# Optimization experiments

Hardware: AMD Instinct MI355X
Metric: run time of the kernel (lower is better)

Reference implementation:

```python
import jax, jax.numpy as jnp
import numpy as np
import math

B, S, E, H, D, L, HF = 8, 1024, 512, 8, 64, 6, 2048
EPS = 1e-5
INF = 1000000.0


def _gelu(x):
    # custom tanh-approx gelu from the source
    return 0.5 * x * (1 + jnp.tanh(math.sqrt(2 / math.pi) * (x + 0.044715 * x ** 3)))


def _layernorm(x, gamma, beta):
    mean = jnp.mean(x, axis=-1, keepdims=True)
    var = jnp.mean((x - mean) ** 2, axis=-1, keepdims=True)
    return gamma * ((x - mean) / jnp.sqrt(var + EPS)) + beta


def setup_inputs() -> dict:
    key = jax.random.key(0)
    ks = jax.random.split(key, 10)
    scale = 0.02
    x = jax.random.normal(ks[0], (B, S, E), dtype=jnp.float32)
    att_mask = jax.random.randint(ks[1], (B, S), 0, 2) == 1
    WQ = jax.random.normal(ks[2], (L, E, E), dtype=jnp.float32) * scale
    WK = jax.random.normal(ks[3], (L, E, E), dtype=jnp.float32) * scale
    WV = jax.random.normal(ks[4], (L, E, E), dtype=jnp.float32) * scale
    WO = jax.random.normal(ks[5], (L, E, E), dtype=jnp.float32) * scale
    W1 = jax.random.normal(ks[6], (L, HF, E), dtype=jnp.float32) * scale
    W2 = jax.random.normal(ks[7], (L, E, HF), dtype=jnp.float32) * scale
    bQ = jnp.zeros((L, E)); bK = jnp.zeros((L, E)); bV = jnp.zeros((L, E)); bO = jnp.zeros((L, E))
    b1 = jnp.zeros((L, HF)); b2 = jnp.zeros((L, E))
    g1 = jnp.ones((L, E)); bt1 = jnp.zeros((L, E))
    g2 = jnp.ones((L, E)); bt2 = jnp.zeros((L, E))
    return {"x": x, "att_mask": att_mask, "WQ": WQ, "bQ": bQ, "WK": WK, "bK": bK,
            "WV": WV, "bV": bV, "WO": WO, "bO": bO, "W1": W1, "b1": b1, "W2": W2,
            "b2": b2, "g1": g1, "bt1": bt1, "g2": g2, "bt2": bt2}


def reference(x, att_mask, WQ, bQ, WK, bK, WV, bV, WO, bO, W1, b1, W2, b2, g1, bt1, g2, bt2):
    # additive mask applied to scores: score - (~mask) * infinity, broadcast over (B,1,1,S)
    inv_att = (~att_mask).astype(x.dtype)[:, None, None, :] * INF
    inv_sqrt_d = 1.0 / math.sqrt(D)
    for l in range(L):
        # --- multi-head self-attention ---
        q = (jnp.einsum('bse,fe->bsf', x, WQ[l]) + bQ[l]).reshape(B, S, H, D).transpose(0, 2, 1, 3)
        k = (jnp.einsum('bse,fe->bsf', x, WK[l]) + bK[l]).reshape(B, S, H, D).transpose(0, 2, 1, 3)
        v = (jnp.einsum('bse,fe->bsf', x, WV[l]) + bV[l]).reshape(B, S, H, D).transpose(0, 2, 1, 3)
        score = jnp.einsum('bhsd,bhtd->bhst', q, k) * inv_sqrt_d - inv_att
        attn = jax.nn.softmax(score, axis=-1)
        o = jnp.einsum('bhst,bhtd->bhsd', attn, v).transpose(0, 2, 1, 3).reshape(B, S, E)
        o = jnp.einsum('bse,fe->bsf', o, WO[l]) + bO[l]
        x = _layernorm(x + o, g1[l], bt1[l])
        # --- pointwise feed-forward ---
        h = _gelu(jnp.einsum('bse,fe->bsf', x, W1[l]) + b1[l])
        f = jnp.einsum('bsf,ef->bse', h, W2[l]) + b2[l]
        x = _layernorm(x + f, g2[l], bt2[l])
    return x
```

## Files before the change

kernel.cpp:

```cpp
#include <hip/hip_runtime.h>
#include <cstdint>
#include <cstddef>

#define NB 8
#define NS 1024
#define NE 512
#define NH 8
#define ND 64
#define NL 6
#define NHF 2048
#define NROW (NB*NS)

typedef __bf16 bf16_t;
typedef __bf16 bf8v __attribute__((ext_vector_type(8)));
typedef __bf16 bf4v __attribute__((ext_vector_type(4)));
typedef float  f4   __attribute__((ext_vector_type(4)));

extern "C" __device__ float __ocml_native_exp2_f32(float);
#define EXP2F __ocml_native_exp2_f32
#define LOG2E 1.4426950408889634f

__device__ __forceinline__ void async_copy16(const bf16_t* g, bf16_t* l) {
    __builtin_amdgcn_global_load_lds(
        (const __attribute__((address_space(1))) void*)g,
        (__attribute__((address_space(3))) void*)l,
        16, 0, 0);
}

__device__ __forceinline__ float gelu_f(float x) {
    const float s = fmaf(0.044715f * x * x, x, x);
    const float e = EXP2F(-2.3022081995f * s);
    return x * __builtin_amdgcn_rcpf(1.0f + e);
}

template<int BN, int ACT, int OUT>
__device__ __forceinline__ void gemm_core(
    bf16_t* __restrict__ sm,
    const bf16_t* __restrict__ A, const bf16_t* __restrict__ Bm,
    const float* __restrict__ bias, bf16_t* __restrict__ Cb,
    int m0, int n0, int N, int K)
{
    constexpr int JN = BN / 32, WSPAN = BN / 2;
    bf16_t* As = sm;
    bf16_t* Bs = sm + 2*128*64;
    const int tid  = threadIdx.x;
    const int lane = tid & 63;
    const int wave = tid >> 6;
    const int wm = wave >> 1, wn = wave & 1;
    const int quad = lane >> 4, l16 = lane & 15;
    const int srow = tid >> 3;
    const int scol = (((tid & 7) ^ (srow & 7)) << 3);

    f4 acc[4][JN] = {};

    const bf16_t* Ag = A  + (size_t)(m0 + srow) * K + scol;
    const bf16_t* Bg = Bm + (size_t)(n0 + srow) * K + scol;
    const int sw = (l16 & 7);

    auto stage = [&](int buf, int kt) {
#pragma unroll
        for (int r = 0; r < 4; ++r)
            async_copy16(Ag + (size_t)r * 32 * K + kt, As + buf*8192 + tid*8 + r*2048);
#pragma unroll
        for (int r = 0; r < BN/32; ++r)
            async_copy16(Bg + (size_t)r * 32 * K + kt, Bs + buf*(BN*64) + tid*8 + r*2048);
    };

    stage(0, 0);
    int buf = 0;
    for (int kt = 0; kt < K; kt += 64, buf ^= 1) {
        __syncthreads();
        if (kt + 64 < K) stage(buf ^ 1, kt + 64);
        const bf16_t* Ab = As + buf*8192;
        const bf16_t* Bb = Bs + buf*(BN*64);
#pragma unroll
        for (int s = 0; s < 2; ++s) {
            const int c8 = ((s*4 + quad) ^ sw) * 8;
            bf8v af[4], bfv[JN];
#pragma unroll
            for (int i = 0; i < 4; ++i)
                af[i] = *(const bf8v*)(Ab + (wm*64 + i*16 + l16)*64 + c8);
#pragma unroll
            for (int j = 0; j < JN; ++j)
                bfv[j] = *(const bf8v*)(Bb + (wn*WSPAN + j*16 + l16)*64 + c8);
#pragma unroll
            for (int i = 0; i < 4; ++i)
#pragma unroll
                for (int j = 0; j < JN; ++j)
                    acc[i][j] = __builtin_amdgcn_mfma_f32_16x16x32_bf16(bfv[j], af[i], acc[i][j], 0, 0, 0);
        }
    }

#pragma unroll
    for (int i = 0; i < 4; ++i) {
        const int mi = m0 + wm*64 + i*16 + l16;
        const size_t m = (size_t)mi;
#pragma unroll
        for (int j = 0; j < JN; ++j) {
            const int nb = n0 + wn*WSPAN + j*16 + quad*4;
            const f4 bv = *(const f4*)(bias + nb);
            f4 v = acc[i][j] + bv;
            if (ACT) {
#pragma unroll
                for (int r = 0; r < 4; ++r) v[r] = gelu_f(v[r]);
            }
            bf4v* cp = (bf4v*)(Cb + m * (size_t)N + nb);
            bf4v o;
            if (OUT == 2) {
                const bf4v old = *cp;
#pragma unroll
                for (int r = 0; r < 4; ++r) o[r] = (bf16_t)((float)old[r] + v[r]);
            } else {
#pragma unroll
                for (int r = 0; r < 4; ++r) o[r] = (bf16_t)v[r];
            }
            *cp = o;
        }
    }
}

template<int BN, int ACT, int OUT>
__global__ __launch_bounds__(256)
void gemm_bt_k(const bf16_t* __restrict__ A, const bf16_t* __restrict__ Bm,
               const float* __restrict__ bias, bf16_t* __restrict__ Cb, int N, int K)
{
    __shared__ __align__(16) bf16_t smem[2*128*64 + 2*BN*64];
    gemm_core<BN, ACT, OUT>(smem, A, Bm, bias, Cb,
                            blockIdx.x * 128, blockIdx.y * BN, N, K);
}

__global__ __launch_bounds__(512, 2)
void gemm_rmw_ln_k(const bf16_t* __restrict__ A, const bf16_t* __restrict__ Bm,
                   const float* __restrict__ bias, bf16_t* __restrict__ xb,
                   const float* __restrict__ gamma, const float* __restrict__ beta,
                   float* __restrict__ fout, int wf, int K)
{
    __shared__ __align__(16) bf16_t As[2*32*64];
    __shared__ __align__(16) bf16_t Bs[2*512*64];
    __shared__ float wsum[8][32], wssq[8][32];
    const int tid  = threadIdx.x;
    const int lane = tid & 63;
    const int wave = tid >> 6;
    const int quad = lane >> 4, l16 = lane & 15;
    const int sw = l16 & 7;
    const int srow = tid >> 3;
    const int scol = ((tid & 7) ^ (srow & 7)) << 3;
    const int m0 = blockIdx.x * 32;

    const bf16_t* Ag = A  + (size_t)(m0 + srow) * K + scol;
    const bf16_t* Bg = Bm + (size_t)srow * K + scol;

    f4 acc[2][4] = {};

    auto stage = [&](int buf, int kt) {
        if (tid < 256)
            async_copy16(Ag + kt, As + buf*2048 + tid*8);
#pragma unroll
        for (int r = 0; r < 8; ++r)
            async_copy16(Bg + (size_t)r * 64 * K + kt, Bs + buf*32768 + (r*512 + tid)*8);
    };

    stage(0, 0);
    int buf = 0;
    for (int kt = 0; kt < K; kt += 64, buf ^= 1) {
        __syncthreads();
        if (kt + 64 < K) stage(buf ^ 1, kt + 64);
        const bf16_t* Ab = As + buf*2048;
        const bf16_t* Bb = Bs + buf*32768;
#pragma unroll
        for (int s = 0; s < 2; ++s) {
            const int c8 = ((s*4 + quad) ^ sw) * 8;
            bf8v af[2], bfv[4];
#pragma unroll
            for (int i = 0; i < 2; ++i)
                af[i] = *(const bf8v*)(Ab + (i*16 + l16)*64 + c8);
#pragma unroll
            for (int j = 0; j < 4; ++j)
                bfv[j] = *(const bf8v*)(Bb + (wave*64 + j*16 + l16)*64 + c8);
#pragma unroll
            for (int i = 0; i < 2; ++i)
#pragma unroll
                for (int j = 0; j < 4; ++j)
                    acc[i][j] = __builtin_amdgcn_mfma_f32_16x16x32_bf16(bfv[j], af[i], acc[i][j], 0, 0, 0);
        }
    }

    f4 v[2][4];
    float ps[2], pss[2];
#pragma unroll
    for (int i = 0; i < 2; ++i) {
        ps[i] = 0.f; pss[i] = 0.f;
        const size_t m = (size_t)(m0 + i*16 + l16);
#pragma unroll
        for (int j = 0; j < 4; ++j) {
            const int nb = wave*64 + j*16 + quad*4;
            const f4 bv = *(const f4*)(bias + nb);
            const bf4v old = *(const bf4v*)(xb + m * NE + nb);
            f4 t = acc[i][j] + bv;
#pragma unroll
            for (int r = 0; r < 4; ++r) {
                t[r] += (float)old[r];
                ps[i]  += t[r];
                pss[i] += t[r] * t[r];
            }
            v[i][j] = t;
        }
        ps[i]  += __shfl_xor(ps[i], 16, 64);
        ps[i]  += __shfl_xor(ps[i], 32, 64);
        pss[i] += __shfl_xor(pss[i], 16, 64);
        pss[i] += __shfl_xor(pss[i], 32, 64);
    }
    if (quad == 0) {
#pragma unroll
        for (int i = 0; i < 2; ++i) {
            wsum[wave][i*16 + l16] = ps[i];
            wssq[wave][i*16 + l16] = pss[i];
        }
    }
    __syncthreads();
#pragma unroll
    for (int i = 0; i < 2; ++i) {
        const int row = i*16 + l16;
        float s = 0.f, ss = 0.f;
#pragma unroll
        for (int w = 0; w < 8; ++w) { s += wsum[w][row]; ss += wssq[w][row]; }
        const float mean = s * (1.0f / NE);
        const float var  = ss * (1.0f / NE) - mean * mean;
        const float inv  = rsqrtf(var + 1e-5f);
        const size_t m = (size_t)(m0 + row);
#pragma unroll
        for (int j = 0; j < 4; ++j) {
            const int nb = wave*64 + j*16 + quad*4;
            const f4 gm = *(const f4*)(gamma + nb);
            const f4 bt = *(const f4*)(beta + nb);
            f4 o;
            bf4v ob;
#pragma unroll
            for (int r = 0; r < 4; ++r) {
                o[r]  = gm[r] * ((v[i][j][r] - mean) * inv) + bt[r];
                ob[r] = (bf16_t)o[r];
            }
            *(bf4v*)(xb + m * NE + nb) = ob;
            if (wf) *(f4*)(fout + m * NE + nb) = o;
        }
    }
}

__global__ __launch_bounds__(256, 2)
void gemm_qkv_k(const bf16_t* __restrict__ A,
                const bf16_t* __restrict__ wq, const bf16_t* __restrict__ wk, const bf16_t* __restrict__ wv,
                const float* __restrict__ bq, const float* __restrict__ bk, const float* __restrict__ bv,
                bf16_t* __restrict__ Q, bf16_t* __restrict__ K, bf16_t* __restrict__ Vt,
                const unsigned short* __restrict__ rank)
{
    __shared__ __align__(16) bf16_t As_[2*128*64];
    __shared__ __align__(16) bf16_t Bs_[3][2*64*64];
    const int tid  = threadIdx.x;
    const int lane = tid & 63;
    const int wave = tid >> 6;
    const int wm = wave >> 1, wn = wave & 1;
    const int quad = lane >> 4, l16 = lane & 15;
    const int sw = l16 & 7;
    const int srow = tid >> 3;
    const int scol = (((tid & 7) ^ (srow & 7)) << 3);
    const int m0 = blockIdx.x * 128, n0 = blockIdx.y * 64;

    const bf16_t* Ag = A + (size_t)(m0 + srow) * NE + scol;
    const bf16_t* Wg0 = wq + (size_t)(n0 + srow) * NE + scol;
    const bf16_t* Wg1 = wk + (size_t)(n0 + srow) * NE + scol;
    const bf16_t* Wg2 = wv + (size_t)(n0 + srow) * NE + scol;

    f4 acc[3][4][2] = {};

    auto stage = [&](int buf, int kt) {
#pragma unroll
        for (int r = 0; r < 4; ++r)
            async_copy16(Ag + (size_t)r*32*NE + kt, As_ + buf*8192 + tid*8 + r*2048);
#pragma unroll
        for (int r = 0; r < 2; ++r) {
            async_copy16(Wg0 + (size_t)r*32*NE + kt, Bs_[0] + buf*4096 + tid*8 + r*2048);
            async_copy16(Wg1 + (size_t)r*32*NE + kt, Bs_[1] + buf*4096 + tid*8 + r*2048);
            async_copy16(Wg2 + (size_t)r*32*NE + kt, Bs_[2] + buf*4096 + tid*8 + r*2048);
        }
    };

    stage(0, 0);
    int buf = 0;
    for (int kt = 0; kt < NE; kt += 64, buf ^= 1) {
        __syncthreads();
        if (kt + 64 < NE) stage(buf ^ 1, kt + 64);
        const bf16_t* Ab = As_ + buf*8192;
#pragma unroll
        for (int s = 0; s < 2; ++s) {
            const int c8 = ((s*4 + quad) ^ sw) * 8;
            bf8v af[4];
#pragma unroll
            for (int i = 0; i < 4; ++i)
                af[i] = *(const bf8v*)(Ab + (wm*64 + i*16 + l16)*64 + c8);
#pragma unroll
            for (int mat = 0; mat < 3; ++mat) {
                const bf16_t* Bb = Bs_[mat] + buf*4096;
                const bf8v b0 = *(const bf8v*)(Bb + (wn*32      + l16)*64 + c8);
                const bf8v b1 = *(const bf8v*)(Bb + (wn*32 + 16 + l16)*64 + c8);
                if (mat < 2) {
#pragma unroll
                    for (int i = 0; i < 4; ++i) {
                        acc[mat][i][0] = __builtin_amdgcn_mfma_f32_16x16x32_bf16(b0, af[i], acc[mat][i][0], 0, 0, 0);
                        acc[mat][i][1] = __builtin_amdgcn_mfma_f32_16x16x32_bf16(b1, af[i], acc[mat][i][1], 0, 0, 0);
                    }
                } else {
#pragma unroll
                    for (int i = 0; i < 4; ++i) {
                        acc[2][i][0] = __builtin_amdgcn_mfma_f32_16x16x32_bf16(af[i], b0, acc[2][i][0], 0, 0, 0);
                        acc[2][i][1] = __builtin_amdgcn_mfma_f32_16x16x32_bf16(af[i], b1, acc[2][i][1], 0, 0, 0);
                    }
                }
            }
        }
    }

#pragma unroll
    for (int i = 0; i < 4; ++i) {
        const int mi = m0 + wm*64 + i*16 + l16;
        const int mk = (mi & ~1023) + (int)rank[mi];
#pragma unroll
        for (int j = 0; j < 2; ++j) {
            const int nb = n0 + wn*32 + j*16 + quad*4;
            const f4 vq = acc[0][i][j] + *(const f4*)(bq + nb);
            const f4 vk = acc[1][i][j] + *(const f4*)(bk + nb);
            bf4v oq, ok;
#pragma unroll
            for (int r = 0; r < 4; ++r) { oq[r] = (bf16_t)vq[r]; ok[r] = (bf16_t)vk[r]; }
            *(bf4v*)(Q + (size_t)mi * NE + nb) = oq;
            *(bf4v*)(K + (size_t)mk * NE + nb) = ok;
        }
    }
#pragma unroll
    for (int j = 0; j < 2; ++j) {
        const int n = n0 + wn*32 + j*16 + l16;
        const float bvv = bv[n];
#pragma unroll
        for (int i = 0; i < 4; ++i) {
            const int mbase = m0 + wm*64 + i*16 + quad*4;
            const size_t b8h = (size_t)((mbase >> 10)*8 + (n >> 6));
            bf16_t* rowp = Vt + (b8h*64 + (size_t)(n & 63))*1024;
#pragma unroll
            for (int r = 0; r < 4; ++r)
                rowp[rank[mbase + r]] = (bf16_t)(acc[2][i][j][r] + bvv);
        }
    }
}

template<int ACT, int OUT>
__device__ __forceinline__ void gemm256_core(
    bf16_t* __restrict__ sm,
    const bf16_t* __restrict__ A, const bf16_t* __restrict__ Bm,
    const float* __restrict__ bias, bf16_t* __restrict__ Cb,
    int m0, int n0, int N, int K)
{
    const int tid  = threadIdx.x;
    const int lane = tid & 63;
    const int wave = tid >> 6;
    const int wm = wave >> 2, wn = wave & 3;
    const int quad = lane >> 4, l16 = lane & 15;
    const int sw = l16 & 7;
    const int srow = tid >> 3;
    const int scol = ((tid & 7) ^ (srow & 7)) << 3;

    bf16_t* As = sm;
    bf16_t* Bs = sm + 4 * 8192;

    const bf16_t* Ag = A  + (size_t)(m0 + srow) * K + scol;
    const bf16_t* Bg = Bm + (size_t)(n0 + srow) * K + scol;

    auto stageA = [&](int d, int h, int kt) {
        bf16_t* dst = As + (d*2 + h) * 8192 + tid * 8;
        const bf16_t* src = Ag + (size_t)(h * 128) * K + kt;
        async_copy16(src, dst);
        async_copy16(src + (size_t)64 * K, dst + 4096);
    };
    auto stageB = [&](int d, int h, int kt) {
        bf16_t* dst = Bs + (d*2 + h) * 8192 + tid * 8;
        const bf16_t* src = Bg + (size_t)(h * 128) * K + kt;
        async_copy16(src, dst);
        async_copy16(src + (size_t)64 * K, dst + 4096);
    };

    const int nt = K >> 6;

    f4 acc[8][4] = {};
    bf8v bfr[4][2], al[4][2], ah[4][2];

    auto mfmaQ = [&](const bf8v (&af)[4][2], int fb, int gb) {
#pragma unroll
        for (int kh = 0; kh < 2; ++kh)
#pragma unroll
            for (int f = 0; f < 4; ++f)
#pragma unroll
                for (int g = 0; g < 2; ++g)
                    acc[fb+f][gb+g] = __builtin_amdgcn_mfma_f32_16x16x32_bf16(bfr[gb+g][kh], af[f][kh], acc[fb+f][gb+g], 0, 0, 0);
    };

    stageB(0, 0, 0);  stageB(0, 1, 0);  stageA(0, 0, 0);  stageA(0, 1, 0);
    stageB(1, 0, 64); stageB(1, 1, 64); stageA(1, 0, 64);
    asm volatile("s_waitcnt vmcnt(6)" ::: "memory");
    __builtin_amdgcn_s_barrier();

    for (int t = 0; t < nt; ++t) {
        const int d = t & 1;
        const int kt2 = (t + 2) << 6;
        const bf16_t* Ab = As + (d*2 + wm) * 8192;
        const bf16_t* Bb = Bs + (d*2 + (wn >> 1)) * 8192 + (wn & 1) * 4096;

#pragma unroll
        for (int g = 0; g < 4; ++g)
#pragma unroll
            for (int kh = 0; kh < 2; ++kh)
                bfr[g][kh] = *(const bf8v*)(Bb + (g*16 + l16)*64 + (((kh*4 + quad) ^ sw) << 3));
#pragma unroll
        for (int f = 0; f < 4; ++f)
#pragma unroll
            for (int kh = 0; kh < 2; ++kh)
                al[f][kh] = *(const bf8v*)(Ab + (f*16 + l16)*64 + (((kh*4 + quad) ^ sw) << 3));
        if (t + 1 < nt) stageA(d ^ 1, 1, (t + 1) << 6);
        __builtin_amdgcn_s_barrier();
        __builtin_amdgcn_s_setprio(1);
        mfmaQ(al, 0, 0);
        __builtin_amdgcn_s_setprio(0);
        asm volatile("s_waitcnt lgkmcnt(0)" ::: "memory");
        __builtin_amdgcn_s_barrier();

#pragma unroll
        for (int f = 0; f < 4; ++f)
#pragma unroll
            for (int kh = 0; kh < 2; ++kh)
                ah[f][kh] = *(const bf8v*)(Ab + ((f + 4)*16 + l16)*64 + (((kh*4 + quad) ^ sw) << 3));
        if (t + 2 < nt) stageB(d, 0, kt2);
        __builtin_amdgcn_s_barrier();
        __builtin_amdgcn_s_setprio(1);
        mfmaQ(ah, 4, 0);
        __builtin_amdgcn_s_setprio(0);
        asm volatile("s_waitcnt lgkmcnt(0)" ::: "memory");
        __builtin_amdgcn_s_barrier();

        if (t + 2 < nt) stageB(d, 1, kt2);
        __builtin_amdgcn_s_barrier();
        __builtin_amdgcn_s_setprio(1);
        mfmaQ(al, 0, 2);
        __builtin_amdgcn_s_setprio(0);
        asm volatile("s_waitcnt lgkmcnt(0)" ::: "memory");
        __builtin_amdgcn_s_barrier();

        if (t + 2 < nt) stageA(d, 0, kt2);
        __builtin_amdgcn_s_barrier();
        __builtin_amdgcn_s_setprio(1);
        mfmaQ(ah, 4, 2);
        __builtin_amdgcn_s_setprio(0);
        asm volatile("s_waitcnt lgkmcnt(0)" ::: "memory");
        if (t + 1 < nt) {
            if (t + 2 < nt) asm volatile("s_waitcnt vmcnt(6)" ::: "memory");
            else            asm volatile("s_waitcnt vmcnt(0)" ::: "memory");
        }
        __builtin_amdgcn_s_barrier();
    }

#pragma unroll
    for (int f = 0; f < 8; ++f) {
        const int mi = m0 + wm*128 + f*16 + l16;
        const size_t m = (size_t)mi;
#pragma unroll
        for (int g = 0; g < 4; ++g) {
            const int nb = n0 + wn*64 + g*16 + quad*4;
            const f4 bv = *(const f4*)(bias + nb);
            f4 v = acc[f][g] + bv;
            if (ACT) {
#pragma unroll
                for (int r = 0; r < 4; ++r) v[r] = gelu_f(v[r]);
            }
            bf4v* cp = (bf4v*)(Cb + m * (size_t)N + nb);
            bf4v o;
            if (OUT == 2) {
                const bf4v old = *cp;
#pragma unroll
                for (int r = 0; r < 4; ++r) o[r] = (bf16_t)((float)old[r] + v[r]);
            } else {
#pragma unroll
                for (int r = 0; r < 4; ++r) o[r] = (bf16_t)v[r];
            }
            *cp = o;
        }
    }
}

template<int ACT, int OUT>
__global__ __launch_bounds__(512, 2)
void gemm256_k(const bf16_t* __restrict__ A, const bf16_t* __restrict__ Bm,
               const float* __restrict__ bias, bf16_t* __restrict__ Cb, int N, int K)
{
    __shared__ __align__(16) bf16_t smem[8 * 8192];
    gemm256_core<ACT, OUT>(smem, A, Bm, bias, Cb,
                           blockIdx.x * 256, blockIdx.y * 256, N, K);
}

__global__ __launch_bounds__(64)
void pack_k(const int* __restrict__ m, unsigned short* __restrict__ rank,
            int* __restrict__ cntpad, float* __restrict__ maskp)
{
    const int b = blockIdx.x, lane = threadIdx.x;
    unsigned long long bals[16];
    int cnt = 0;
#pragma unroll
    for (int c = 0; c < 16; ++c) {
        const bool mk = m[b*NS + c*64 + lane] != 0;
        bals[c] = __ballot(mk);
        cnt += __popcll(bals[c]);
    }
    int u = 0, kk = 0;
#pragma unroll
    for (int c = 0; c < 16; ++c) {
        const unsigned long long bal = bals[c];
        const bool mk = (bal >> lane) & 1;
        const int pu = __popcll(bal & ((1ull << lane) - 1));
        const int r = mk ? (u + pu) : (cnt + kk + (lane - pu));
        rank[b*NS + c*64 + lane] = (unsigned short)r;
        const int cb = __popcll(bal);
        u += cb; kk += 64 - cb;
    }
    if (lane == 0) {
        int cp = (cnt + 63) & ~63;
        cntpad[b] = cp < 64 ? 64 : cp;
    }
#pragma unroll
    for (int c = 0; c < 16; ++c) {
        const int j = c*64 + lane;
        maskp[b*NS + j] = (j < cnt) ? 0.0f : -1.0e6f * LOG2E;
    }
}

__global__ __launch_bounds__(256)
void attn_k(const bf16_t* __restrict__ Q, const bf16_t* __restrict__ Kg,
            const bf16_t* __restrict__ Vt, const float* __restrict__ maskf,
            const int* __restrict__ cntpad, bf16_t* __restrict__ O)
{
    __shared__ __align__(16) bf16_t Ks[2][64*64];
    __shared__ __align__(16) bf16_t Vs[2][64*64];
    __shared__ __align__(16) bf16_t Ps[4][32*64];
    const int tid  = threadIdx.x;
    const int lane = tid & 63;
    const int wave = tid >> 6;
    const int quad = lane >> 4, l16 = lane & 15;
    const int sw = l16 & 7;
    const int bh = blockIdx.x;
    const int b = bh >> 3, h = bh & 7;
    const int q0 = blockIdx.y * 128;
    const int kend = cntpad[b];

    bf8v qf[2][2];
#pragma unroll
    for (int qi = 0; qi < 2; ++qi) {
        const bf16_t* Qp = Q + (size_t)(b*NS + q0 + wave*32 + qi*16 + l16) * NE + h*ND;
        qf[qi][0] = *(const bf8v*)(Qp + quad*8);
        qf[qi][1] = *(const bf8v*)(Qp + 32 + quad*8);
    }

    f4 oacc[2][4] = {};
    float rs[2] = {0.f, 0.f};

    const int srow = tid >> 3;
    const int scol = (((tid & 7) ^ (srow & 7)) << 3);
    const float c1 = 0.125f * LOG2E;

    auto stage = [&](int buf, int kt) {
#pragma unroll
        for (int r = 0; r < 2; ++r) {
            async_copy16(Kg + (size_t)(b*NS + kt + r*32 + srow) * NE + h*ND + scol,
                         Ks[buf] + (r*256 + tid) * 8);
            async_copy16(Vt + (size_t)(bh*ND + r*32 + srow) * NS + kt + scol,
                         Vs[buf] + (r*256 + tid) * 8);
        }
    };

    stage(0, 0);
    int buf = 0;
    for (int kt = 0; kt < kend; kt += 64, buf ^= 1) {
        __syncthreads();
        if (kt + 64 < kend) stage(buf ^ 1, kt + 64);

        f4 sacc[2][4] = {};
        __builtin_amdgcn_s_setprio(1);
#pragma unroll
        for (int j = 0; j < 4; ++j) {
            bf8v kf0 = *(const bf8v*)(Ks[buf] + (j*16 + l16)*64 + ((quad    ) ^ sw)*8);
            bf8v kf1 = *(const bf8v*)(Ks[buf] + (j*16 + l16)*64 + ((quad + 4) ^ sw)*8);
#pragma unroll
            for (int qi = 0; qi < 2; ++qi) {
                sacc[qi][j] = __builtin_amdgcn_mfma_f32_16x16x32_bf16(kf0, qf[qi][0], sacc[qi][j], 0, 0, 0);
                sacc[qi][j] = __builtin_amdgcn_mfma_f32_16x16x32_bf16(kf1, qf[qi][1], sacc[qi][j], 0, 0, 0);
            }
        }
        __builtin_amdgcn_s_setprio(0);

        bf16_t* Pw = Ps[wave];
#pragma unroll
        for (int j = 0; j < 4; ++j) {
            const f4 mkv = *(const f4*)(maskf + b*NS + kt + j*16 + quad*4);
#pragma unroll
            for (int qi = 0; qi < 2; ++qi) {
                bf4v o;
#pragma unroll
                for (int r = 0; r < 4; ++r) {
                    const float p = EXP2F(fmaf(sacc[qi][j][r], c1, mkv[r]));
                    rs[qi] += p;
                    o[r] = (bf16_t)p;
                }
                const int row = qi*16 + l16;
                const int chunk = (j*2 + (quad >> 1)) ^ sw;
                *(bf4v*)(Pw + row*64 + chunk*8 + (quad & 1)*4) = o;
            }
        }

        __builtin_amdgcn_s_setprio(1);
#pragma unroll
        for (int ks = 0; ks < 2; ++ks) {
            bf8v pf[2];
#pragma unroll
            for (int qi = 0; qi < 2; ++qi)
                pf[qi] = *(const bf8v*)(Pw + (qi*16 + l16)*64 + ((ks*4 + quad) ^ sw)*8);
#pragma unroll
            for (int nt = 0; nt < 4; ++nt) {
                bf8v vf = *(const bf8v*)(Vs[buf] + (nt*16 + l16)*64 + ((ks*4 + quad) ^ sw)*8);
#pragma unroll
                for (int qi = 0; qi < 2; ++qi)
                    oacc[qi][nt] = __builtin_amdgcn_mfma_f32_16x16x32_bf16(vf, pf[qi], oacc[qi][nt], 0, 0, 0);
            }
        }
        __builtin_amdgcn_s_setprio(0);
    }

#pragma unroll
    for (int qi = 0; qi < 2; ++qi) {
        float s = rs[qi];
        s += __shfl_xor(s, 16, 64);
        s += __shfl_xor(s, 32, 64);
        const float inv = 1.0f / s;
        const size_t row = (size_t)(b*NS + q0 + wave*32 + qi*16 + l16);
#pragma unroll
        for (int nt = 0; nt < 4; ++nt) {
            bf4v o;
#pragma unroll
            for (int r = 0; r < 4; ++r) o[r] = (bf16_t)(oacc[qi][nt][r] * inv);
            *(bf4v*)(O + row * NE + h*ND + nt*16 + quad*4) = o;
        }
    }
}

__global__ __launch_bounds__(256)
void ln_k(bf16_t* __restrict__ xb,
          const float* __restrict__ gamma, const float* __restrict__ beta,
          float* __restrict__ fout, int wf)
{
    const int row = blockIdx.x;
    const int tid = threadIdx.x;
    const size_t base = (size_t)row * NE;
    const float x0 = (float)xb[base + tid];
    const float x1 = (float)xb[base + tid + 256];
    float s  = x0 + x1;
    float ss = x0*x0 + x1*x1;
#pragma unroll
    for (int off = 32; off > 0; off >>= 1) {
        s  += __shfl_down(s,  off, 64);
        ss += __shfl_down(ss, off, 64);
    }
    __shared__ float red[8];
    const int wave = tid >> 6;
    if ((tid & 63) == 0) { red[wave] = s; red[4 + wave] = ss; }
    __syncthreads();
    s  = red[0] + red[1] + red[2] + red[3];
    ss = red[4] + red[5] + red[6] + red[7];
    const float mean = s * (1.0f / NE);
    const float var  = ss * (1.0f / NE) - mean * mean;
    const float inv  = rsqrtf(var + 1e-5f);
    const float o0 = gamma[tid]       * ((x0 - mean) * inv) + beta[tid];
    const float o1 = gamma[tid + 256] * ((x1 - mean) * inv) + beta[tid + 256];
    xb[base + tid]       = (bf16_t)o0;
    xb[base + tid + 256] = (bf16_t)o1;
    if (wf) {
        fout[base + tid]       = o0;
        fout[base + tid + 256] = o1;
    }
}

#define W4SZ ((size_t)NL*NE*NE/4)
#define WBSZ ((size_t)NL*NE*NHF/4)
#define XSZ  ((size_t)NROW*NE/4)
#define CVT_TOTAL (4*W4SZ + 2*WBSZ + XSZ)

__global__ void cvt_all(const float* __restrict__ wq, const float* __restrict__ wk,
                        const float* __restrict__ wv, const float* __restrict__ wo,
                        const float* __restrict__ w1, const float* __restrict__ w2,
                        const float* __restrict__ x,
                        bf16_t* __restrict__ owq, bf16_t* __restrict__ owk,
                        bf16_t* __restrict__ owv, bf16_t* __restrict__ owo,
                        bf16_t* __restrict__ ow1, bf16_t* __restrict__ ow2,
                        bf16_t* __restrict__ ox)
{
    size_t i = (size_t)blockIdx.x * 256 + threadIdx.x;
    if (i >= CVT_TOTAL) return;
    const float* src; bf16_t* dst;
    if      (i < 1*W4SZ)           { src = wq; dst = owq; }
    else if (i < 2*W4SZ)           { src = wk; dst = owk; i -= 1*W4SZ; }
    else if (i < 3*W4SZ)           { src = wv; dst = owv; i -= 2*W4SZ; }
    else if (i < 4*W4SZ)           { src = wo; dst = owo; i -= 3*W4SZ; }
    else if (i < 4*W4SZ + WBSZ)    { src = w1; dst = ow1; i -= 4*W4SZ; }
    else if (i < 4*W4SZ + 2*WBSZ)  { src = w2; dst = ow2; i -= 4*W4SZ + WBSZ; }
    else                           { src = x;  dst = ox;  i -= 4*W4SZ + 2*WBSZ; }
    const f4 v = ((const f4*)src)[i];
    bf4v o;
    o[0] = (bf16_t)v[0]; o[1] = (bf16_t)v[1]; o[2] = (bf16_t)v[2]; o[3] = (bf16_t)v[3];
    ((bf4v*)dst)[i] = o;
}

extern "C" void kernel_launch(void* const* d_in, const int* in_sizes, int n_in,
                              void* d_out, int out_size, void* d_ws, size_t ws_size,
                              hipStream_t stream)
{
    (void)in_sizes; (void)n_in; (void)out_size; (void)ws_size;
    const float* x   = (const float*)d_in[0];
    const int*   msk = (const int*)d_in[1];
    const float* WQ = (const float*)d_in[2];  const float* bQ  = (const float*)d_in[3];
    const float* WK = (const float*)d_in[4];  const float* bK  = (const float*)d_in[5];
    const float* WV = (const float*)d_in[6];  const float* bV  = (const float*)d_in[7];
    const float* WO = (const float*)d_in[8];  const float* bO  = (const float*)d_in[9];
    const float* W1 = (const float*)d_in[10]; const float* b1  = (const float*)d_in[11];
    const float* W2 = (const float*)d_in[12]; const float* b2  = (const float*)d_in[13];
    const float* g1 = (const float*)d_in[14]; const float* bt1 = (const float*)d_in[15];
    const float* g2 = (const float*)d_in[16]; const float* bt2 = (const float*)d_in[17];

    char* ws = (char*)d_ws;
    size_t off = 0;
    auto alloc = [&](size_t bytes) { char* p = ws + off; off += (bytes + 255) & ~(size_t)255; return p; };
    bf16_t* xb    = (bf16_t*)alloc((size_t)NROW*NE*2);
    bf16_t* Qb    = (bf16_t*)alloc((size_t)NROW*NE*2);
    bf16_t* Kb    = (bf16_t*)alloc((size_t)NROW*NE*2);
    bf16_t* Vtb   = (bf16_t*)alloc((size_t)NROW*NE*2);
    bf16_t* AOb   = (bf16_t*)alloc((size_t)NROW*NE*2);
    bf16_t* hb    = (bf16_t*)alloc((size_t)NROW*NHF*2);
    bf16_t* wqc   = (bf16_t*)alloc((size_t)NL*NE*NE*2);
    bf16_t* wkc   = (bf16_t*)alloc((size_t)NL*NE*NE*2);
    bf16_t* wvc   = (bf16_t*)alloc((size_t)NL*NE*NE*2);
    bf16_t* woc   = (bf16_t*)alloc((size_t)NL*NE*NE*2);
    bf16_t* w1c   = (bf16_t*)alloc((size_t)NL*NHF*NE*2);
    bf16_t* w2c   = (bf16_t*)alloc((size_t)NL*NE*NHF*2);
    float*  maskp = (float*) alloc((size_t)NB*NS*4);
    unsigned short* rankb = (unsigned short*)alloc((size_t)NB*NS*2);
    int*    cntp  = (int*)   alloc(NB*4);

    cvt_all<<<dim3((unsigned)((CVT_TOTAL + 255) / 256)), dim3(256), 0, stream>>>(
        WQ, WK, WV, WO, W1, W2, x, wqc, wkc, wvc, woc, w1c, w2c, xb);
    pack_k<<<dim3(NB), dim3(64), 0, stream>>>(msk, rankb, cntp, maskp);

    for (int l = 0; l < NL; ++l) {
        const bf16_t* wq  = wqc + (size_t)l*NE*NE;
        const bf16_t* wk  = wkc + (size_t)l*NE*NE;
        const bf16_t* wv  = wvc + (size_t)l*NE*NE;
        const bf16_t* wo  = woc + (size_t)l*NE*NE;
        const bf16_t* w1p = w1c + (size_t)l*NHF*NE;
        const bf16_t* w2p = w2c + (size_t)l*NE*NHF;
        const int last = (l == NL - 1);

        gemm_qkv_k<<<dim3(64, 8), dim3(256), 0, stream>>>(
            xb, wq, wk, wv, bQ + l*NE, bK + l*NE, bV + l*NE, Qb, Kb, Vtb, rankb);
        attn_k<<<dim3(64, 8), dim3(256), 0, stream>>>(Qb, Kb, Vtb, maskp, cntp, AOb);
        gemm_rmw_ln_k<<<dim3(256), dim3(512), 0, stream>>>(
            AOb, wo, bO + l*NE, xb, g1 + l*NE, bt1 + l*NE,
            nullptr, 0, NE);
        gemm256_k<1, 1><<<dim3(32, 8), dim3(512), 0, stream>>>(
            xb, w1p, b1 + l*NHF, hb, NHF, NE);
        gemm_bt_k<128, 0, 2><<<dim3(64, 4), dim3(256), 0, stream>>>(
            hb, w2p, b2 + l*NE, xb, NE, NHF);
        ln_k<<<dim3(NROW), dim3(256), 0, stream>>>(
            xb, g2 + l*NE, bt2 + l*NE, (float*)d_out, last);
    }
}
```

Baseline: 916.3 us.

## Fuse second LayerNorm into FFN2 GEMM via last-block atomic counter

Drops the separate ln_k launch and folds the post-FFN LayerNorm into the FFN2 GEMM kernel. Each of the four N-tile blocks of a 128-row stripe bumps a per-layer atomic counter, and the last one to arrive normalizes those 128 rows with one wave per row. This removes a kernel launch and a full extra read-modify-write of xb. In exchange it adds threadfences and an atomic, and the LN tail runs on only a quarter of the blocks. Counters are zeroed in pack_k.

Measured after the change: 1.232 ms. 34.4% more time.

```diff
diff --git a/kernel.cpp b/kernel.cpp
--- a/kernel.cpp
+++ b/kernel.cpp
@@ -119,14 +119,59 @@
     }
 }
 
-template<int BN, int ACT, int OUT>
 __global__ __launch_bounds__(256)
-void gemm_bt_k(const bf16_t* __restrict__ A, const bf16_t* __restrict__ Bm,
-               const float* __restrict__ bias, bf16_t* __restrict__ Cb, int N, int K)
-{
-    __shared__ __align__(16) bf16_t smem[2*128*64 + 2*BN*64];
-    gemm_core<BN, ACT, OUT>(smem, A, Bm, bias, Cb,
-                            blockIdx.x * 128, blockIdx.y * BN, N, K);
+void gemm_ffn2_ln_k(const bf16_t* __restrict__ A, const bf16_t* __restrict__ Bm,
+                    const float* __restrict__ bias, bf16_t* __restrict__ xb,
+                    const float* __restrict__ gamma, const float* __restrict__ beta,
+                    float* __restrict__ fout, int wf, int K, int* __restrict__ ctr)
+{
+    __shared__ __align__(16) bf16_t smem[2*128*64 + 2*128*64];
+    gemm_core<128, 0, 2>(smem, A, Bm, bias, xb,
+                         blockIdx.x * 128, blockIdx.y * 128, NE, K);
+
+    __threadfence();
+    __shared__ int go_s;
+    if (threadIdx.x == 0)
+        go_s = (atomicAdd(ctr + blockIdx.x, 1) == 3) ? 1 : 0;
+    __syncthreads();
+    if (!go_s) return;
+    __threadfence();
+
+    const int wave = threadIdx.x >> 6, lane = threadIdx.x & 63;
+    const f4 g0 = *(const f4*)(gamma + lane*8);
+    const f4 g1 = *(const f4*)(gamma + lane*8 + 4);
+    const f4 b0 = *(const f4*)(beta  + lane*8);
+    const f4 b1 = *(const f4*)(beta  + lane*8 + 4);
+    for (int rr = 0; rr < 32; ++rr) {
+        const size_t row  = (size_t)blockIdx.x * 128 + wave * 32 + rr;
+        const size_t base = row * NE;
+        const bf8v v = *(const bf8v*)(xb + base + lane*8);
+        float xv[8], s = 0.f, ss = 0.f;
+#pragma unroll
+        for (int r = 0; r < 8; ++r) { xv[r] = (float)v[r]; s += xv[r]; ss += xv[r]*xv[r]; }
+#pragma unroll
+        for (int off = 32; off > 0; off >>= 1) {
+            s  += __shfl_xor(s,  off, 64);
+            ss += __shfl_xor(ss, off, 64);
+        }
+        const float mean = s * (1.0f / NE);
+        const float var  = ss * (1.0f / NE) - mean * mean;
+        const float inv  = rsqrtf(var + 1e-5f);
+        f4 o0, o1;
+        bf8v ob;
+#pragma unroll
+        for (int r = 0; r < 4; ++r) {
+            o0[r] = g0[r] * ((xv[r]     - mean) * inv) + b0[r];
+            o1[r] = g1[r] * ((xv[r + 4] - mean) * inv) + b1[r];
+            ob[r]     = (bf16_t)o0[r];
+            ob[r + 4] = (bf16_t)o1[r];
+        }
+        *(bf8v*)(xb + base + lane*8) = ob;
+        if (wf) {
+            *(f4*)(fout + base + lane*8)     = o0;
+            *(f4*)(fout + base + lane*8 + 4) = o1;
+        }
+    }
 }
 
 __global__ __launch_bounds__(512, 2)
@@ -504,9 +549,13 @@
 
 __global__ __launch_bounds__(64)
 void pack_k(const int* __restrict__ m, unsigned short* __restrict__ rank,
-            int* __restrict__ cntpad, float* __restrict__ maskp)
+            int* __restrict__ cntpad, float* __restrict__ maskp,
+            int* __restrict__ ctr)
 {
     const int b = blockIdx.x, lane = threadIdx.x;
+#pragma unroll
+    for (int i = lane; i < NL*64/NB; i += 64)
+        ctr[b*(NL*64/NB) + i] = 0;
     unsigned long long bals[16];
     int cnt = 0;
 #pragma unroll
@@ -651,42 +700,6 @@
             for (int r = 0; r < 4; ++r) o[r] = (bf16_t)(oacc[qi][nt][r] * inv);
             *(bf4v*)(O + row * NE + h*ND + nt*16 + quad*4) = o;
         }
-    }
-}
-
-__global__ __launch_bounds__(256)
-void ln_k(bf16_t* __restrict__ xb,
-          const float* __restrict__ gamma, const float* __restrict__ beta,
-          float* __restrict__ fout, int wf)
-{
-    const int row = blockIdx.x;
-    const int tid = threadIdx.x;
-    const size_t base = (size_t)row * NE;
-    const float x0 = (float)xb[base + tid];
-    const float x1 = (float)xb[base + tid + 256];
-    float s  = x0 + x1;
-    float ss = x0*x0 + x1*x1;
-#pragma unroll
-    for (int off = 32; off > 0; off >>= 1) {
-        s  += __shfl_down(s,  off, 64);
-        ss += __shfl_down(ss, off, 64);
-    }
-    __shared__ float red[8];
-    const int wave = tid >> 6;
-    if ((tid & 63) == 0) { red[wave] = s; red[4 + wave] = ss; }
-    __syncthreads();
-    s  = red[0] + red[1] + red[2] + red[3];
-    ss = red[4] + red[5] + red[6] + red[7];
-    const float mean = s * (1.0f / NE);
-    const float var  = ss * (1.0f / NE) - mean * mean;
-    const float inv  = rsqrtf(var + 1e-5f);
-    const float o0 = gamma[tid]       * ((x0 - mean) * inv) + beta[tid];
-    const float o1 = gamma[tid + 256] * ((x1 - mean) * inv) + beta[tid + 256];
-    xb[base + tid]       = (bf16_t)o0;
-    xb[base + tid + 256] = (bf16_t)o1;
-    if (wf) {
-        fout[base + tid]       = o0;
-        fout[base + tid + 256] = o1;
     }
 }
 
@@ -754,10 +767,11 @@
     float*  maskp = (float*) alloc((size_t)NB*NS*4);
     unsigned short* rankb = (unsigned short*)alloc((size_t)NB*NS*2);
     int*    cntp  = (int*)   alloc(NB*4);
+    int*    ctrb  = (int*)   alloc((size_t)NL*64*4);
 
     cvt_all<<<dim3((unsigned)((CVT_TOTAL + 255) / 256)), dim3(256), 0, stream>>>(
         WQ, WK, WV, WO, W1, W2, x, wqc, wkc, wvc, woc, w1c, w2c, xb);
-    pack_k<<<dim3(NB), dim3(64), 0, stream>>>(msk, rankb, cntp, maskp);
+    pack_k<<<dim3(NB), dim3(64), 0, stream>>>(msk, rankb, cntp, maskp, ctrb);
 
     for (int l = 0; l < NL; ++l) {
         const bf16_t* wq  = wqc + (size_t)l*NE*NE;
@@ -776,9 +790,8 @@
             nullptr, 0, NE);
         gemm256_k<1, 1><<<dim3(32, 8), dim3(512), 0, stream>>>(
             xb, w1p, b1 + l*NHF, hb, NHF, NE);
-        gemm_bt_k<128, 0, 2><<<dim3(64, 4), dim3(256), 0, stream>>>(
-            hb, w2p, b2 + l*NE, xb, NE, NHF);
-        ln_k<<<dim3(NROW), dim3(256), 0, stream>>>(
-            xb, g2 + l*NE, bt2 + l*NE, (float*)d_out, last);
-    }
-}
+        gemm_ffn2_ln_k<<<dim3(64, 4), dim3(256), 0, stream>>>(
+            hb, w2p, b2 + l*NE, xb, g2 + l*NE, bt2 + l*NE,
+            (float*)d_out, last, NHF, ctrb + l*64);
+    }
+}
```
